# Optimization experiments

Hardware: AMD Instinct MI355X
Metric: run time of the kernel (lower is better)

## Reference

```python
import jax, jax.numpy as jnp
import numpy as np
from jax import lax
from jax.scipy.special import logsumexp

B, L, D = 64, 256, 512
NUM_CLASS, NREF, NNEG = 10, 50, 100
BLUR = 0.05
EPS_FINAL = BLUR ** 2  # geomloss: eps = blur**p with p=2
MARGIN = 10.0

# epsilon-scaling schedule (geomloss anneals eps geometrically, scaling=0.5),
# then extra iterations at the final eps for convergence.
_sched = []
_e = 8.0
while _e > EPS_FINAL:
    _sched.append(_e)
    _e *= 0.5
_sched += [EPS_FINAL] * 15
EPS_SCHED = jnp.asarray(np.array(_sched, np.float32))


def _cost(x, y):
    # geomloss p=2 cost: |x - y|^2 / 2   -> [N, M]
    return 0.5 * (jnp.sum(x * x, -1)[:, None] + jnp.sum(y * y, -1)[None, :] - 2.0 * (x @ y.T))


def _ot(a, x, b, y):
    """Entropic OT value <a,f>+<b,g> via log-domain Sinkhorn with eps-scaling.
    a,b are (possibly zero-padded) weights; x,y point clouds."""
    C = _cost(x, y)
    loga = jnp.where(a > 0, jnp.log(jnp.maximum(a, 1e-30)), -1e9)
    logb = jnp.where(b > 0, jnp.log(jnp.maximum(b, 1e-30)), -1e9)

    def body(fg, eps):
        f, g = fg
        f = -eps * logsumexp(logb[None, :] + (g[None, :] - C) / eps, axis=1)
        g = -eps * logsumexp(loga[:, None] + (f[:, None] - C) / eps, axis=0)
        return (f, g), None

    (f, g), _ = lax.scan(body, (jnp.zeros_like(a), jnp.zeros_like(b)), EPS_SCHED)
    return jnp.sum(a * f) + jnp.sum(b * g)


def _forward(anchor, weight, anchor_out_neg, t0, grade, grade_neg):
    Cn = t0.shape[0]
    w_ref = jnp.full((t0.shape[1],), 1.0 / t0.shape[1], anchor.dtype)
    w_neg = jnp.full((anchor_out_neg.shape[1],), 1.0 / anchor_out_neg.shape[1], anchor.dtype)

    # cross OT anchor_i vs every class reference cloud: [B, C]
    ot_cross = jax.vmap(lambda a, x: jax.vmap(lambda y: _ot(a, x, w_ref, y))(t0))(weight, anchor)
    # self terms for debiasing
    ot_aa = jax.vmap(lambda a, x: _ot(a, x, a, x))(weight, anchor)            # [B]
    ot_tt = jax.vmap(lambda y: _ot(w_ref, y, w_ref, y))(t0)                    # [C]
    ot_nn = jax.vmap(lambda y: _ot(w_neg, y, w_neg, y))(anchor_out_neg)        # [B]

    # debiased Sinkhorn divergence S = OT_ab - 0.5 OT_aa - 0.5 OT_bb
    S = ot_cross - 0.5 * ot_aa[:, None] - 0.5 * ot_tt[None, :]                 # [B, C]
    pos = jnp.take_along_axis(S, grade[:, None], axis=1)[:, 0]                 # [B]

    # after the torch k-loop, k == num_class-1 (loop-variable leak) -> t0[last]
    t_last = t0[Cn - 1]
    ot_ln = jax.vmap(lambda y: _ot(w_ref, t_last, w_neg, y))(anchor_out_neg)   # [B]
    S_last = ot_ln - 0.5 * ot_tt[Cn - 1] - 0.5 * ot_nn

    t_g = t0[grade_neg]                                                        # [B, NREF, D]
    ot_gn = jax.vmap(lambda yt, yn: _ot(w_ref, yt, w_neg, yn))(t_g, anchor_out_neg)
    S_gn = ot_gn - 0.5 * ot_tt[grade_neg] - 0.5 * ot_nn

    # hinge over all classes k != grade[i], plus the neg-cloud entry (index -1)
    notself = jnp.arange(Cn)[None, :] != grade[:, None]
    hinge_cls = jnp.sum(jnp.where(notself, jax.nn.relu(pos[:, None] - S + MARGIN), 0.0), axis=1)
    hinge_neg = jax.nn.relu(pos - S_last + MARGIN)
    loss_dif = jnp.abs(S_gn - S_last)
    return jnp.mean(hinge_cls + hinge_neg + loss_dif)


def setup_inputs() -> dict:
    key = jax.random.key(0)
    ks = jax.random.split(key, 7)
    anchor = jax.random.normal(ks[0], (B, L, D), jnp.float32)
    length_anchor = jax.random.randint(ks[1], (B,), L // 2, L + 1)
    grade = jax.random.randint(ks[2], (B,), 0, NUM_CLASS)
    w = jax.random.uniform(ks[3], (B, L), jnp.float32, 1e-3, 1.0)
    mask = jnp.arange(L)[None, :] < length_anchor[:, None]
    w = w * mask
    weight = w / jnp.sum(w, axis=1, keepdims=True)  # normalized histogram per sample
    anchor_out_neg = jax.random.normal(ks[4], (B, NNEG, D), jnp.float32)
    grade_neg = jax.random.randint(ks[5], (B,), 0, NUM_CLASS)
    t0 = jax.random.normal(ks[6], (NUM_CLASS, NREF, D), jnp.float32)
    return {"anchor": anchor, "length_anchor": length_anchor, "grade": grade,
            "weight": weight, "anchor_out_neg": anchor_out_neg,
            "grade_neg": grade_neg, "t0": t0, "num_class": NUM_CLASS}


def reference(anchor, length_anchor, grade, weight, anchor_out_neg, grade_neg, t0, num_class):
    # length_anchor is encoded in the zero-padding of `weight` (masked positions
    # have weight 0 and drop out of the OT); num_class == t0.shape[0].
    return _forward(anchor, weight, anchor_out_neg, t0, grade, grade_neg)
```

## Files before the change

### kernel.cpp

```cpp
#include <hip/hip_runtime.h>

#define NB   64
#define LA   256
#define DD   512
#define NCLS 10
#define NREF 50
#define NNEG 100
#define MARGIN 10.0f
#define NITER 27

#define LOG2E 1.44269504f
#define LN2   0.69314718f
#define LC50  (-3.9120230054f)
#define LC100 (-4.6051701860f)

#define OFF_CX   ((size_t)0)
#define SZ_CX    ((size_t)64*500*256)
#define OFF_CAA  (OFF_CX + SZ_CX)
#define SZ_CAA   ((size_t)64*256*256)
#define OFF_CNN  (OFF_CAA + SZ_CAA)
#define SZ_CNN   ((size_t)64*100*100)
#define OFF_CLN  (OFF_CNN + SZ_CNN)
#define SZ_CLN   ((size_t)64*50*100)
#define OFF_CGN  (OFF_CLN + SZ_CLN)
#define SZ_CGN   ((size_t)64*50*100)
#define OFF_CTT  (OFF_CGN + SZ_CGN)
#define SZ_CTT   ((size_t)10*50*50)
#define OFF_SQA  (OFF_CTT + SZ_CTT)
#define OFF_SQN  (OFF_SQA + (size_t)64*256)
#define OFF_SQT  (OFF_SQN + (size_t)64*100)
#define OFF_OTX  (OFF_SQT + (size_t)500)
#define OFF_OTAA (OFF_OTX + (size_t)640)
#define OFF_OTNN (OFF_OTAA + (size_t)64)
#define OFF_OTLN (OFF_OTNN + (size_t)64)
#define OFF_OTGN (OFF_OTLN + (size_t)64)
#define OFF_OTTT (OFF_OTGN + (size_t)64)

__device__ __forceinline__ float eps_at(int it) {
    return (it < 12) ? ldexpf(8.0f, -it) : 0.0025f;
}

__global__ __launch_bounds__(256) void sq_kernel(const float* __restrict__ anchor,
                                                 const float* __restrict__ neg,
                                                 const float* __restrict__ t0,
                                                 float* __restrict__ ws) {
    int gw   = (blockIdx.x * 256 + threadIdx.x) >> 6;
    int lane = threadIdx.x & 63;
    const int nA = NB * LA, nN = NB * NNEG, nT = NCLS * NREF;
    if (gw >= nA + nN + nT) return;
    const float* row; float* outp;
    if (gw < nA)           { row = anchor + (size_t)gw * DD;          outp = ws + OFF_SQA + gw; }
    else if (gw < nA + nN) { int r = gw - nA;      row = neg + (size_t)r * DD; outp = ws + OFF_SQN + r; }
    else                   { int r = gw - nA - nN; row = t0  + (size_t)r * DD; outp = ws + OFF_SQT + r; }
    const float4* r4 = (const float4*)row;
    float4 u = r4[lane * 2], v = r4[lane * 2 + 1];
    float s = u.x*u.x + u.y*u.y + u.z*u.z + u.w*u.w
            + v.x*v.x + v.y*v.y + v.z*v.z + v.w*v.w;
    #pragma unroll
    for (int off = 1; off < 64; off <<= 1) s += __shfl_xor(s, off);
    if (lane == 0) *outp = 0.5f * s;
}

#define CTM 128
#define CTK 16
__global__ __launch_bounds__(256) void cost128(const float* __restrict__ anchor,
                                               const float* __restrict__ neg,
                                               const float* __restrict__ t0,
                                               const int* __restrict__ gneg,
                                               float* __restrict__ ws) {
    __shared__ __align__(16) float As[CTK][CTM];
    __shared__ __align__(16) float Bs[CTK][CTM];
    int bid = blockIdx.x, tid = threadIdx.x;
    const float *X, *Y, *sqx, *sqy;
    float* Cout; int N, M, ldc, r0, c0;
    bool tr = false;
    if (bid < 512) {
        int b = bid >> 3, t = bid & 7;
        r0 = (t >> 2) * 128; c0 = (t & 3) * 128;
        X = anchor + (size_t)b * LA * DD; Y = t0; N = LA; M = 500; ldc = 500;
        Cout = ws + OFF_CX + (size_t)b * 500 * 256;
        sqx = ws + OFF_SQA + b * LA; sqy = ws + OFF_SQT;
        tr = true;
    } else if (bid < 768) {
        int b2 = bid - 512; int b = b2 >> 2, t = b2 & 3;
        r0 = (t >> 1) * 128; c0 = (t & 1) * 128;
        X = Y = anchor + (size_t)b * LA * DD; N = M = LA; ldc = LA;
        Cout = ws + OFF_CAA + (size_t)b * LA * LA;
        sqx = sqy = ws + OFF_SQA + b * LA;
    } else if (bid < 832) {
        int b = bid - 768; r0 = 0; c0 = 0;
        X = Y = neg + (size_t)b * NNEG * DD; N = M = NNEG; ldc = NNEG;
        Cout = ws + OFF_CNN + (size_t)b * NNEG * NNEG;
        sqx = sqy = ws + OFF_SQN + b * NNEG;
    } else if (bid < 896) {
        int b = bid - 832; r0 = 0; c0 = 0;
        X = t0 + (size_t)9 * NREF * DD; Y = neg + (size_t)b * NNEG * DD;
        N = NREF; M = NNEG; ldc = NNEG;
        Cout = ws + OFF_CLN + (size_t)b * NREF * NNEG;
        sqx = ws + OFF_SQT + 9 * NREF; sqy = ws + OFF_SQN + b * NNEG;
    } else if (bid < 960) {
        int b = bid - 896; r0 = 0; c0 = 0;
        int gc = gneg[b];
        X = t0 + (size_t)gc * NREF * DD; Y = neg + (size_t)b * NNEG * DD;
        N = NREF; M = NNEG; ldc = NNEG;
        Cout = ws + OFF_CGN + (size_t)b * NREF * NNEG;
        sqx = ws + OFF_SQT + gc * NREF; sqy = ws + OFF_SQN + b * NNEG;
    } else {
        int c = bid - 960; r0 = 0; c0 = 0;
        X = Y = t0 + (size_t)c * NREF * DD; N = M = NREF; ldc = NREF;
        Cout = ws + OFF_CTT + (size_t)c * NREF * NREF;
        sqx = sqy = ws + OFF_SQT + c * NREF;
    }
    int row = tid & 127, kq = tid >> 7;
    int tx = tid & 15, ty = tid >> 4;
    bool xok = (r0 + row) < N, yok = (c0 + row) < M;
    const float* xrow = X + (size_t)(r0 + row) * DD + kq * 8;
    const float* yrow = Y + (size_t)(c0 + row) * DD + kq * 8;
    float acc[8][8];
    #pragma unroll
    for (int a = 0; a < 8; a++)
        #pragma unroll
        for (int b = 0; b < 8; b++) acc[a][b] = 0.f;
    for (int k0 = 0; k0 < DD; k0 += CTK) {
        float4 xa0 = xok ? *(const float4*)(xrow + k0)     : make_float4(0,0,0,0);
        float4 xa1 = xok ? *(const float4*)(xrow + k0 + 4) : make_float4(0,0,0,0);
        float4 ya0 = yok ? *(const float4*)(yrow + k0)     : make_float4(0,0,0,0);
        float4 ya1 = yok ? *(const float4*)(yrow + k0 + 4) : make_float4(0,0,0,0);
        __syncthreads();
        int kb = kq * 8;
        As[kb+0][row]=xa0.x; As[kb+1][row]=xa0.y; As[kb+2][row]=xa0.z; As[kb+3][row]=xa0.w;
        As[kb+4][row]=xa1.x; As[kb+5][row]=xa1.y; As[kb+6][row]=xa1.z; As[kb+7][row]=xa1.w;
        Bs[kb+0][row]=ya0.x; Bs[kb+1][row]=ya0.y; Bs[kb+2][row]=ya0.z; Bs[kb+3][row]=ya0.w;
        Bs[kb+4][row]=ya1.x; Bs[kb+5][row]=ya1.y; Bs[kb+6][row]=ya1.z; Bs[kb+7][row]=ya1.w;
        __syncthreads();
        #pragma unroll
        for (int k = 0; k < CTK; k++) {
            float4 a0 = *(const float4*)&As[k][ty << 3];
            float4 a1 = *(const float4*)&As[k][(ty << 3) + 4];
            float4 b0 = *(const float4*)&Bs[k][tx << 3];
            float4 b1 = *(const float4*)&Bs[k][(tx << 3) + 4];
            float av[8] = {a0.x,a0.y,a0.z,a0.w,a1.x,a1.y,a1.z,a1.w};
            float bv[8] = {b0.x,b0.y,b0.z,b0.w,b1.x,b1.y,b1.z,b1.w};
            #pragma unroll
            for (int a = 0; a < 8; a++)
                #pragma unroll
                for (int b = 0; b < 8; b++)
                    acc[a][b] = fmaf(av[a], bv[b], acc[a][b]);
        }
    }
    #pragma unroll
    for (int a = 0; a < 8; a++) {
        int n = r0 + (ty << 3) + a;
        if (n < N) {
            float sx = sqx[n];
            #pragma unroll
            for (int b = 0; b < 8; b++) {
                int m = c0 + (tx << 3) + b;
                if (m < M) {
                    float v = sx + sqy[m] - acc[a][b];
                    if (tr) Cout[(size_t)m * 256 + n] = v;
                    else    Cout[(size_t)n * ldc + m] = v;
                }
            }
        }
    }
}

__global__ __launch_bounds__(1024) void sink_fused(const float* __restrict__ weight,
                                                   float* __restrict__ ws) {
    __shared__ __align__(16) float smem[26664];
    int bid = blockIdx.x, tid = threadIdx.x;

    if (bid < 64) {
        float* ahp = smem;
        float* red = smem + 1024;
        int w = tid >> 6, lane = tid & 63;
        int c = (w << 4) | (lane & 15);
        int rg = lane >> 4;
        const float* Cg = ws + OFF_CAA + ((size_t)bid << 16);
        float Creg[64];
        #pragma unroll
        for (int k = 0; k < 64; ++k)
            Creg[k] = Cg[(size_t)((rg << 6) + k) * 256 + c];
        float wgt = weight[(size_t)bid * LA + c];
        float la = (wgt > 0.f) ? __logf(fmaxf(wgt, 1e-30f)) : -1e9f;
        float h = 0.f, fs = 0.f;
        int wseg = (c >> 6) * 68 + (c & 63);
        if (rg == 0) ahp[wseg] = 8.0f * la;
        __syncthreads();
        for (int app = 0; app < 54; ++app) {
            float eps = eps_at(app >> 1);
            const float4* a4 = (const float4*)(ahp + (app & 1) * 272 + rg * 68);
            float m0=-3.4e38f, m1=-3.4e38f, m2=-3.4e38f, m3=-3.4e38f;
            #pragma unroll
            for (int k = 0; k < 16; ++k) {
                float4 av = a4[k];
                m0 = fmaxf(m0, av.x - Creg[4*k+0]);
                m1 = fmaxf(m1, av.y - Creg[4*k+1]);
                m2 = fmaxf(m2, av.z - Creg[4*k+2]);
                m3 = fmaxf(m3, av.w - Creg[4*k+3]);
            }
            float m = fmaxf(fmaxf(m0, m1), fmaxf(m2, m3));
            m = fmaxf(m, __shfl_xor(m, 16));
            m = fmaxf(m, __shfl_xor(m, 32));
            float ie2 = (1.0f / eps) * LOG2E;
            float s0=0.f, s1=0.f, s2=0.f, s3=0.f;
            #pragma unroll
            for (int k = 0; k < 16; ++k) {
                float4 av = a4[k];
                s0 += exp2f((av.x - Creg[4*k+0] - m) * ie2);
                s1 += exp2f((av.y - Creg[4*k+1] - m) * ie2);
                s2 += exp2f((av.z - Creg[4*k+2] - m) * ie2);
                s3 += exp2f((av.w - Creg[4*k+3] - m) * ie2);
            }
            float s = (s0 + s1) + (s2 + s3);
            s += __shfl_xor(s, 16);
            s += __shfl_xor(s, 32);
            h = -fmaf(eps * LN2, __log2f(s), m);
            if (app == 52) fs = h;
            float epsn = eps_at((app + 1) >> 1);
            if (rg == 0) ahp[((app + 1) & 1) * 272 + wseg] = fmaf(epsn, la, h);
            __syncthreads();
        }
        float contrib = (rg == 0) ? wgt * (fs + h) : 0.f;
        #pragma unroll
        for (int off = 1; off < 64; off <<= 1) contrib += __shfl_xor(contrib, off);
        if (lane == 0) red[w] = contrib;
        __syncthreads();
        if (tid == 0) {
            float s = 0.f;
            #pragma unroll
            for (int k = 0; k < 16; ++k) s += red[k];
            ws[OFF_OTAA + bid] = s;
        }

    } else if (bid < 80) {
        int sub = tid >> 8, stid = tid & 255;
        int inst = ((bid - 64) << 2) | sub;
        const float* Cg = ws + OFF_CNN + (size_t)inst * 10000;
        float* S = smem + (sub << 8);
        bool act = stid < 200;
        int c = stid >> 1, rg = stid & 1;
        float Creg[52];
        if (act) {
            #pragma unroll
            for (int k = 0; k < 52; ++k) {
                int r = rg * 52 + k;
                Creg[k] = (r < 100) ? Cg[(size_t)r * 100 + c] : 3.0e30f;
            }
        }
        if (stid < 100) S[stid] = 8.0f * LC100;
        if (stid >= 100 && stid < 104) { S[stid] = -1.0e30f; S[104 + stid] = -1.0e30f; }
        __syncthreads();
        float h = 0.f, fs = 0.f;
        for (int app = 0; app < 54; ++app) {
            float eps = eps_at(app >> 1);
            if (act) {
                const float4* a4 = (const float4*)(S + (app & 1) * 104 + rg * 52);
                float m0=-3.4e38f, m1=-3.4e38f, m2=-3.4e38f, m3=-3.4e38f;
                #pragma unroll
                for (int k = 0; k < 13; ++k) {
                    float4 av = a4[k];
                    m0 = fmaxf(m0, av.x - Creg[4*k+0]);
                    m1 = fmaxf(m1, av.y - Creg[4*k+1]);
                    m2 = fmaxf(m2, av.z - Creg[4*k+2]);
                    m3 = fmaxf(m3, av.w - Creg[4*k+3]);
                }
                float m = fmaxf(fmaxf(m0, m1), fmaxf(m2, m3));
                m = fmaxf(m, __shfl_xor(m, 1));
                float ie2 = (1.0f / eps) * LOG2E;
                float s0=0.f, s1=0.f, s2=0.f, s3=0.f;
                #pragma unroll
                for (int k = 0; k < 13; ++k) {
                    float4 av = a4[k];
                    s0 += exp2f((av.x - Creg[4*k+0] - m) * ie2);
                    s1 += exp2f((av.y - Creg[4*k+1] - m) * ie2);
                    s2 += exp2f((av.z - Creg[4*k+2] - m) * ie2);
                    s3 += exp2f((av.w - Creg[4*k+3] - m) * ie2);
                }
                float s = (s0 + s1) + (s2 + s3);
                s += __shfl_xor(s, 1);
                h = -fmaf(eps * LN2, __log2f(s), m);
                if (app == 52) fs = h;
                float epsn = eps_at((app + 1) >> 1);
                if (rg == 0) S[((app + 1) & 1) * 104 + c] = fmaf(epsn, LC100, h);
            }
            __syncthreads();
        }
        float contrib = (act && rg == 0) ? 0.01f * (fs + h) : 0.f;
        #pragma unroll
        for (int off = 1; off < 64; off <<= 1) contrib += __shfl_xor(contrib, off);
        if ((tid & 63) == 0) smem[1024 + (tid >> 6)] = contrib;
        __syncthreads();
        if (stid == 0) {
            int b4 = 1024 + (sub << 2);
            ws[OFF_OTNN + inst] = smem[b4] + smem[b4+1] + smem[b4+2] + smem[b4+3];
        }

    } else if (bid < 112) {
        int sub = tid >> 8, stid = tid & 255;
        int inst = ((bid - 80) << 2) | sub;
        const float* Cg = (inst < 64) ? ws + OFF_CLN + (size_t)inst * 5000
                                      : ws + OFF_CGN + (size_t)(inst - 64) * 5000;
        float* outp = (inst < 64) ? ws + OFF_OTLN + inst : ws + OFF_OTGN + (inst - 64);
        float* S = smem + (sub << 8);
        float* gS = S;
        float* fS = S + 104;
        bool actf = stid < 100; int rf = stid >> 1, hf = stid & 1;
        bool actg = (stid >= 128) && (stid < 228); int cg = stid - 128;
        float Creg[52];
        if (actf) {
            #pragma unroll
            for (int k = 0; k < 52; ++k) {
                int cc = hf * 52 + k;
                Creg[k] = (cc < 100) ? Cg[(size_t)rf * 100 + cc] : 3.0e30f;
            }
        } else if (actg) {
            #pragma unroll
            for (int k = 0; k < 52; ++k)
                Creg[k] = (k < 50) ? Cg[(size_t)k * 100 + cg] : 3.0e30f;
        }
        if (stid < 104) gS[stid] = (stid < 100) ? 8.0f * LC100 : -1.0e30f;
        if (stid == 0) { fS[50] = -1.0e30f; fS[51] = -1.0e30f; }
        __syncthreads();
        float fr = 0.f, gr = 0.f;
        for (int it = 0; it < NITER; ++it) {
            float eps = eps_at(it), ie2 = (1.0f / eps) * LOG2E;
            if (actf) {
                const float4* g4 = (const float4*)(gS + hf * 52);
                float m0=-3.4e38f, m1=-3.4e38f, m2=-3.4e38f, m3=-3.4e38f;
                #pragma unroll
                for (int k = 0; k < 13; ++k) {
                    float4 gv = g4[k];
                    m0 = fmaxf(m0, gv.x - Creg[4*k+0]);
                    m1 = fmaxf(m1, gv.y - Creg[4*k+1]);
                    m2 = fmaxf(m2, gv.z - Creg[4*k+2]);
                    m3 = fmaxf(m3, gv.w - Creg[4*k+3]);
                }
                float m = fmaxf(fmaxf(m0, m1), fmaxf(m2, m3));
                m = fmaxf(m, __shfl_xor(m, 1));
                float s0=0.f, s1=0.f, s2=0.f, s3=0.f;
                #pragma unroll
                for (int k = 0; k < 13; ++k) {
                    float4 gv = g4[k];
                    s0 += exp2f((gv.x - Creg[4*k+0] - m) * ie2);
                    s1 += exp2f((gv.y - Creg[4*k+1] - m) * ie2);
                    s2 += exp2f((gv.z - Creg[4*k+2] - m) * ie2);
                    s3 += exp2f((gv.w - Creg[4*k+3] - m) * ie2);
                }
                float s = (s0 + s1) + (s2 + s3);
                s += __shfl_xor(s, 1);
                fr = -fmaf(eps * LN2, __log2f(s), m);
                if (hf == 0) fS[rf] = fmaf(eps, LC50, fr);
            }
            __syncthreads();
            if (actg) {
                const float4* f4 = (const float4*)fS;
                float m0=-3.4e38f, m1=-3.4e38f, m2=-3.4e38f, m3=-3.4e38f;
                #pragma unroll
                for (int k = 0; k < 13; ++k) {
                    float4 fv = f4[k];
                    m0 = fmaxf(m0, fv.x - Creg[4*k+0]);
                    m1 = fmaxf(m1, fv.y - Creg[4*k+1]);
                    m2 = fmaxf(m2, fv.z - Creg[4*k+2]);
                    m3 = fmaxf(m3, fv.w - Creg[4*k+3]);
                }
                float m = fmaxf(fmaxf(m0, m1), fmaxf(m2, m3));
                float s0=0.f, s1=0.f, s2=0.f, s3=0.f;
                #pragma unroll
                for (int k = 0; k < 13; ++k) {
                    float4 fv = f4[k];
                    s0 += exp2f((fv.x - Creg[4*k+0] - m) * ie2);
                    s1 += exp2f((fv.y - Creg[4*k+1] - m) * ie2);
                    s2 += exp2f((fv.z - Creg[4*k+2] - m) * ie2);
                    s3 += exp2f((fv.w - Creg[4*k+3] - m) * ie2);
                }
                gr = -fmaf(eps * LN2, __log2f((s0+s1)+(s2+s3)), m);
                float epsn = eps_at(it + 1);
                gS[cg] = fmaf(epsn, LC100, gr);
            }
            __syncthreads();
        }
        float contrib = 0.f;
        if (actf && hf == 0) contrib += 0.02f * fr;
        if (actg) contrib += 0.01f * gr;
        #pragma unroll
        for (int off = 1; off < 64; off <<= 1) contrib += __shfl_xor(contrib, off);
        if ((tid & 63) == 0) smem[1024 + (tid >> 6)] = contrib;
        __syncthreads();
        if (stid == 0) {
            int b4 = 1024 + (sub << 2);
            *outp = smem[b4] + smem[b4+1] + smem[b4+2] + smem[b4+3];
        }

    } else if (bid < 115) {
        int sub = tid >> 8, stid = tid & 255;
        int inst = ((bid - 112) << 2) | sub;
        bool live = inst < 10;
        const float* Cg = ws + OFF_CTT + (size_t)inst * 2500;
        float* S = smem + (sub << 8);
        bool act = live && (stid < 50);
        float Creg[52];
        if (act) {
            #pragma unroll
            for (int k = 0; k < 52; ++k)
                Creg[k] = (k < 50) ? Cg[(size_t)k * 50 + stid] : 3.0e30f;
        }
        if (live && stid < 50) S[stid] = 8.0f * LC50;
        if (live && stid >= 50 && stid < 52) { S[stid] = -1.0e30f; S[52 + stid] = -1.0e30f; }
        __syncthreads();
        float h = 0.f, fs = 0.f;
        for (int app = 0; app < 54; ++app) {
            float eps = eps_at(app >> 1);
            if (act) {
                const float4* a4 = (const float4*)(S + (app & 1) * 52);
                float m0=-3.4e38f, m1=-3.4e38f, m2=-3.4e38f, m3=-3.4e38f;
                #pragma unroll
                for (int k = 0; k < 13; ++k) {
                    float4 av = a4[k];
                    m0 = fmaxf(m0, av.x - Creg[4*k+0]);
                    m1 = fmaxf(m1, av.y - Creg[4*k+1]);
                    m2 = fmaxf(m2, av.z - Creg[4*k+2]);
                    m3 = fmaxf(m3, av.w - Creg[4*k+3]);
                }
                float m = fmaxf(fmaxf(m0, m1), fmaxf(m2, m3));
                float ie2 = (1.0f / eps) * LOG2E;
                float s0=0.f, s1=0.f, s2=0.f, s3=0.f;
                #pragma unroll
                for (int k = 0; k < 13; ++k) {
                    float4 av = a4[k];
                    s0 += exp2f((av.x - Creg[4*k+0] - m) * ie2);
                    s1 += exp2f((av.y - Creg[4*k+1] - m) * ie2);
                    s2 += exp2f((av.z - Creg[4*k+2] - m) * ie2);
                    s3 += exp2f((av.w - Creg[4*k+3] - m) * ie2);
                }
                h = -fmaf(eps * LN2, __log2f((s0+s1)+(s2+s3)), m);
                if (app == 52) fs = h;
                float epsn = eps_at((app + 1) >> 1);
                S[((app + 1) & 1) * 52 + stid] = fmaf(epsn, LC50, h);
            }
            __syncthreads();
        }
        float contrib = act ? 0.02f * (fs + h) : 0.f;
        #pragma unroll
        for (int off = 1; off < 64; off <<= 1) contrib += __shfl_xor(contrib, off);
        if ((tid & 63) == 0) smem[1024 + (tid >> 6)] = contrib;
        __syncthreads();
        if (stid == 0 && live) {
            int b4 = 1024 + (sub << 2);
            ws[OFF_OTTT + inst] = smem[b4] + smem[b4+1] + smem[b4+2] + smem[b4+3];
        }

    } else {
        int sub = tid >> 9, stid = tid & 511;
        int inst = ((bid - 115) << 1) | sub;
        int i = inst / 10, c = inst - i * 10;
        float* base = smem + sub * 13324;
        float* CsT = base;
        float* agS = base + 13000;
        float* gSp = base + 13260;
        float* red = smem + 26648;
        const float* Cgbase = ws + OFF_CX + (size_t)i * (500 * 256) + (size_t)c * (50 * 256);
        bool wk = stid < 256;
        if (wk) {
            for (int e = stid; e < 3200; e += 256) {
                int r = e >> 6, n4 = (e & 63) << 2;
                *(float4*)&CsT[r * 260 + n4] = *(const float4*)&Cgbase[(size_t)e << 2];
            }
        }
        float w = 0.f, la_r = 0.f;
        if (wk) {
            w = weight[(size_t)i * LA + stid];
            la_r = (w > 0.f) ? __logf(fmaxf(w, 1e-30f)) : -1e9f;
            if (stid < 52) gSp[stid] = (stid < 50) ? 0.f : -1.0e30f;
        }
        __syncthreads();
        int grp = stid >> 4, j = stid & 15;
        for (int it = 0; it < NITER; ++it) {
            float eps = eps_at(it), ie2 = (1.0f / eps) * LOG2E;
            if (wk) {
                float m0=-3.4e38f, m1=-3.4e38f, m2=-3.4e38f, m3=-3.4e38f;
                #pragma unroll
                for (int r = 0; r < 48; r += 4) {
                    m0 = fmaxf(m0, gSp[r+0] - CsT[(r+0)*260 + stid]);
                    m1 = fmaxf(m1, gSp[r+1] - CsT[(r+1)*260 + stid]);
                    m2 = fmaxf(m2, gSp[r+2] - CsT[(r+2)*260 + stid]);
                    m3 = fmaxf(m3, gSp[r+3] - CsT[(r+3)*260 + stid]);
                }
                m0 = fmaxf(m0, gSp[48] - CsT[48*260 + stid]);
                m1 = fmaxf(m1, gSp[49] - CsT[49*260 + stid]);
                float m = fmaxf(fmaxf(m0, m1), fmaxf(m2, m3));
                float s0=0.f, s1=0.f, s2=0.f, s3=0.f;
                #pragma unroll
                for (int r = 0; r < 48; r += 4) {
                    s0 += exp2f((gSp[r+0] - CsT[(r+0)*260 + stid] - m) * ie2);
                    s1 += exp2f((gSp[r+1] - CsT[(r+1)*260 + stid] - m) * ie2);
                    s2 += exp2f((gSp[r+2] - CsT[(r+2)*260 + stid] - m) * ie2);
                    s3 += exp2f((gSp[r+3] - CsT[(r+3)*260 + stid] - m) * ie2);
                }
                s0 += exp2f((gSp[48] - CsT[48*260 + stid] - m) * ie2);
                s1 += exp2f((gSp[49] - CsT[49*260 + stid] - m) * ie2);
                float L = fmaf(eps * LN2, __log2f((s0+s1)+(s2+s3)), m);
                float f = -fmaf(eps, LC50, L);
                agS[stid] = fmaf(eps, la_r, f);
            }
            __syncthreads();
            if (wk) {
                float4 agr[4];
                #pragma unroll
                for (int q = 0; q < 4; ++q)
                    agr[q] = *(const float4*)&agS[(j << 2) + (q << 6)];
                for (int o = grp; o < 50; o += 16) {
                    const float* Cr = &CsT[o * 260];
                    float u[16];
                    #pragma unroll
                    for (int q = 0; q < 4; ++q) {
                        float4 cv = *(const float4*)&Cr[(j << 2) + (q << 6)];
                        u[4*q+0] = agr[q].x - cv.x;
                        u[4*q+1] = agr[q].y - cv.y;
                        u[4*q+2] = agr[q].z - cv.z;
                        u[4*q+3] = agr[q].w - cv.w;
                    }
                    float a0 = fmaxf(fmaxf(u[0], u[4]),  fmaxf(u[8],  u[12]));
                    float a1 = fmaxf(fmaxf(u[1], u[5]),  fmaxf(u[9],  u[13]));
                    float a2 = fmaxf(fmaxf(u[2], u[6]),  fmaxf(u[10], u[14]));
                    float a3 = fmaxf(fmaxf(u[3], u[7]),  fmaxf(u[11], u[15]));
                    float m = fmaxf(fmaxf(a0, a1), fmaxf(a2, a3));
                    #pragma unroll
                    for (int off = 1; off < 16; off <<= 1) m = fmaxf(m, __shfl_xor(m, off));
                    float s0=0.f, s1=0.f, s2=0.f, s3=0.f;
                    #pragma unroll
                    for (int k = 0; k < 16; ++k) {
                        float e = exp2f((u[k] - m) * ie2);
                        if ((k & 3) == 0) s0 += e;
                        else if ((k & 3) == 1) s1 += e;
                        else if ((k & 3) == 2) s2 += e;
                        else s3 += e;
                    }
                    float s = (s0 + s1) + (s2 + s3);
                    #pragma unroll
                    for (int off = 1; off < 16; off <<= 1) s += __shfl_xor(s, off);
                    if (j == 0) gSp[o] = -fmaf(eps * LN2, __log2f(s), m);
                }
            }
            __syncthreads();
        }
        float contrib = 0.f;
        if (wk) {
            float f_t = agS[stid] - 0.0025f * la_r;
            contrib = w * f_t + (stid < 50 ? 0.02f * gSp[stid] : 0.f);
        }
        #pragma unroll
        for (int off = 1; off < 64; off <<= 1) contrib += __shfl_xor(contrib, off);
        if ((tid & 63) == 0) red[tid >> 6] = contrib;
        __syncthreads();
        if (stid == 0) {
            int b8 = sub << 3;
            float s = 0.f;
            #pragma unroll
            for (int k = 0; k < 4; ++k) s += red[b8 + k];
            ws[OFF_OTX + inst] = s;
        }
    }
}

__global__ void assemble_kernel(const int* __restrict__ grade, const int* __restrict__ gneg,
                                const float* __restrict__ ws, float* __restrict__ out) {
    int i = threadIdx.x;
    float total = 0.f;
    if (i < 64) {
        float aa  = ws[OFF_OTAA + i];
        float nn  = ws[OFF_OTNN + i];
        float lnv = ws[OFF_OTLN + i];
        float gnv = ws[OFF_OTGN + i];
        int g  = grade[i];
        int gi = gneg[i];
        float tt9 = ws[OFF_OTTT + 9];
        float ttg = ws[OFF_OTTT + gi];
        float Slast = lnv - 0.5f * tt9 - 0.5f * nn;
        float Sgn   = gnv - 0.5f * ttg - 0.5f * nn;
        float Sv[10];
        #pragma unroll
        for (int k = 0; k < 10; k++)
            Sv[k] = ws[OFF_OTX + i * 10 + k] - 0.5f * aa - 0.5f * ws[OFF_OTTT + k];
        float pos = 0.f;
        #pragma unroll
        for (int k = 0; k < 10; k++) pos = (k == g) ? Sv[k] : pos;
        float hc = 0.f;
        #pragma unroll
        for (int k = 0; k < 10; k++)
            if (k != g) hc += fmaxf(pos - Sv[k] + MARGIN, 0.f);
        float hn = fmaxf(pos - Slast + MARGIN, 0.f);
        total = hc + hn + fabsf(Sgn - Slast);
    }
    #pragma unroll
    for (int off = 1; off < 64; off <<= 1) total += __shfl_xor(total, off);
    if (i == 0) out[0] = total * (1.0f / 64.0f);
}

extern "C" void kernel_launch(void* const* d_in, const int* in_sizes, int n_in,
                              void* d_out, int out_size, void* d_ws, size_t ws_size,
                              hipStream_t stream) {
    const float* anchor = (const float*)d_in[0];
    const int*   grade  = (const int*)d_in[2];
    const float* weight = (const float*)d_in[3];
    const float* neg    = (const float*)d_in[4];
    const int*   gneg   = (const int*)d_in[5];
    const float* t0     = (const float*)d_in[6];
    float* ws  = (float*)d_ws;
    float* out = (float*)d_out;

    sq_kernel      <<<5821, 256, 0, stream>>>(anchor, neg, t0, ws);
    cost128        <<<970, 256, 0, stream>>>(anchor, neg, t0, gneg, ws);
    sink_fused     <<<435, 1024, 0, stream>>>(weight, ws);
    assemble_kernel<<<1, 64, 0, stream>>>(grade, gneg, ws, out);
}
```

Measured before the change: 594.0 us.

## Remap self-OT threads so shared potential reads broadcast, reduce partials via LDS

Changes the thread mapping in the anchor self-OT Sinkhorn blocks so that each wave covers 64 consecutive columns and all lanes of a wave read the same row potentials, which turns shared-memory reads into broadcasts. Cross-row-group reductions now go through shared-memory partial arrays and extra barriers instead of wave shuffles, and the double-buffered padded potential array becomes a single buffer. The aim is to cut LDS traffic and bank conflicts in the inner loop, at the cost of two additional __syncthreads per half-iteration.

New measurement: 597.9 us. No clear change (+0.7%).

```diff
diff --git a/kernel.cpp b/kernel.cpp
--- a/kernel.cpp
+++ b/kernel.cpp
@@ -172,57 +172,58 @@
     int bid = blockIdx.x, tid = threadIdx.x;
 
     if (bid < 64) {
-        float* ahp = smem;
-        float* red = smem + 1024;
+        float* ahS = smem;
+        float* pm  = smem + 256;
+        float* ps  = smem + 1296;
+        float* red = smem + 2336;
         int w = tid >> 6, lane = tid & 63;
-        int c = (w << 4) | (lane & 15);
-        int rg = lane >> 4;
+        int q = w >> 2;
+        int c = ((w & 3) << 6) | lane;
         const float* Cg = ws + OFF_CAA + ((size_t)bid << 16);
         float Creg[64];
         #pragma unroll
         for (int k = 0; k < 64; ++k)
-            Creg[k] = Cg[(size_t)((rg << 6) + k) * 256 + c];
+            Creg[k] = Cg[(size_t)((q << 6) + k) * 256 + c];
         float wgt = weight[(size_t)bid * LA + c];
         float la = (wgt > 0.f) ? __logf(fmaxf(wgt, 1e-30f)) : -1e9f;
         float h = 0.f, fs = 0.f;
-        int wseg = (c >> 6) * 68 + (c & 63);
-        if (rg == 0) ahp[wseg] = 8.0f * la;
-        __syncthreads();
+        if (q == 0) ahS[c] = 8.0f * la;
+        __syncthreads();
+        int rbase = q << 6;
         for (int app = 0; app < 54; ++app) {
             float eps = eps_at(app >> 1);
-            const float4* a4 = (const float4*)(ahp + (app & 1) * 272 + rg * 68);
-            float m0=-3.4e38f, m1=-3.4e38f, m2=-3.4e38f, m3=-3.4e38f;
-            #pragma unroll
-            for (int k = 0; k < 16; ++k) {
-                float4 av = a4[k];
-                m0 = fmaxf(m0, av.x - Creg[4*k+0]);
-                m1 = fmaxf(m1, av.y - Creg[4*k+1]);
-                m2 = fmaxf(m2, av.z - Creg[4*k+2]);
-                m3 = fmaxf(m3, av.w - Creg[4*k+3]);
-            }
-            float m = fmaxf(fmaxf(m0, m1), fmaxf(m2, m3));
-            m = fmaxf(m, __shfl_xor(m, 16));
-            m = fmaxf(m, __shfl_xor(m, 32));
+            float m0 = -3.4e38f, m1 = -3.4e38f, m2 = -3.4e38f, m3 = -3.4e38f;
+            #pragma unroll
+            for (int k = 0; k < 64; k += 4) {
+                m0 = fmaxf(m0, ahS[rbase + k + 0] - Creg[k + 0]);
+                m1 = fmaxf(m1, ahS[rbase + k + 1] - Creg[k + 1]);
+                m2 = fmaxf(m2, ahS[rbase + k + 2] - Creg[k + 2]);
+                m3 = fmaxf(m3, ahS[rbase + k + 3] - Creg[k + 3]);
+            }
+            pm[q * 260 + c] = fmaxf(fmaxf(m0, m1), fmaxf(m2, m3));
+            __syncthreads();
+            float m = fmaxf(fmaxf(pm[c], pm[260 + c]), fmaxf(pm[520 + c], pm[780 + c]));
             float ie2 = (1.0f / eps) * LOG2E;
-            float s0=0.f, s1=0.f, s2=0.f, s3=0.f;
-            #pragma unroll
-            for (int k = 0; k < 16; ++k) {
-                float4 av = a4[k];
-                s0 += exp2f((av.x - Creg[4*k+0] - m) * ie2);
-                s1 += exp2f((av.y - Creg[4*k+1] - m) * ie2);
-                s2 += exp2f((av.z - Creg[4*k+2] - m) * ie2);
-                s3 += exp2f((av.w - Creg[4*k+3] - m) * ie2);
-            }
-            float s = (s0 + s1) + (s2 + s3);
-            s += __shfl_xor(s, 16);
-            s += __shfl_xor(s, 32);
+            float s0 = 0.f, s1 = 0.f, s2 = 0.f, s3 = 0.f;
+            #pragma unroll
+            for (int k = 0; k < 64; k += 4) {
+                s0 += exp2f((ahS[rbase + k + 0] - Creg[k + 0] - m) * ie2);
+                s1 += exp2f((ahS[rbase + k + 1] - Creg[k + 1] - m) * ie2);
+                s2 += exp2f((ahS[rbase + k + 2] - Creg[k + 2] - m) * ie2);
+                s3 += exp2f((ahS[rbase + k + 3] - Creg[k + 3] - m) * ie2);
+            }
+            ps[q * 260 + c] = (s0 + s1) + (s2 + s3);
+            __syncthreads();
+            float s = (ps[c] + ps[260 + c]) + (ps[520 + c] + ps[780 + c]);
             h = -fmaf(eps * LN2, __log2f(s), m);
             if (app == 52) fs = h;
-            float epsn = eps_at((app + 1) >> 1);
-            if (rg == 0) ahp[((app + 1) & 1) * 272 + wseg] = fmaf(epsn, la, h);
-            __syncthreads();
-        }
-        float contrib = (rg == 0) ? wgt * (fs + h) : 0.f;
+            if (q == 0) {
+                float epsn = eps_at((app + 1) >> 1);
+                ahS[c] = fmaf(epsn, la, h);
+            }
+            __syncthreads();
+        }
+        float contrib = (q == 0) ? wgt * (fs + h) : 0.f;
         #pragma unroll
         for (int off = 1; off < 64; off <<= 1) contrib += __shfl_xor(contrib, off);
         if (lane == 0) red[w] = contrib;
```
